# Kernel tuning notes

Measured on AMD Instinct MI355X. Metric: run time of the kernel, lower is better.

Reference implementation:

```python
import jax, jax.numpy as jnp
import numpy as np

MEMORY_LENGTH = 32   # past states remembered
N_TARGETS = 3        # leak sources
T_STEPS = 1000       # duration / dt
DT = 0.1
HIDDEN = 128         # policy MLP hidden width
N_AGENTS = 1024      # vmapped batch of rollouts
IN_DIM = MEMORY_LENGTH * 3 + MEMORY_LENGTH  # flattened x_hist + conc_hist


def setup_inputs() -> dict:
    key = jax.random.key(0)
    k0, k1, k2, k3, k4 = jax.random.split(key, 5)
    target_pos = jax.random.normal(k0, (N_TARGETS, 2), dtype=jnp.float32) * 5.0
    logsigma = jax.random.normal(k1, (N_TARGETS,), dtype=jnp.float32) * 0.5
    x_inits = jax.random.normal(k2, (N_AGENTS, 3), dtype=jnp.float32) * 2.0
    W1 = jax.random.normal(k3, (HIDDEN, IN_DIM), dtype=jnp.float32) / np.sqrt(IN_DIM).astype(np.float32)
    b1 = jnp.zeros((HIDDEN,), dtype=jnp.float32)
    W2 = jax.random.normal(k4, (2, HIDDEN), dtype=jnp.float32) / np.sqrt(HIDDEN).astype(np.float32)
    b2 = jnp.zeros((2,), dtype=jnp.float32)
    return {"target_pos": target_pos, "logsigma": logsigma, "x_inits": x_inits,
            "W1": W1, "b1": b1, "W2": W2, "b2": b2}


def _concentration(x, y, target_pos, sigma):
    # x, y: [N]; target_pos: [nt, 2]; sigma: [nt] -> conc: [N]
    d2 = (x[:, None] - target_pos[None, :, 0]) ** 2 + (y[:, None] - target_pos[None, :, 1]) ** 2
    return ((1.0 / sigma) * jnp.exp(-d2 / sigma)).sum(-1)


def reference(target_pos, logsigma, x_inits, W1, b1, W2, b2):
    sigma = jnp.exp(logsigma)
    N = x_inits.shape[0]
    # initial histories: memory_length copies of the initial state / concentration
    x_hist0 = jnp.tile(x_inits[:, None, :], (1, MEMORY_LENGTH, 1))        # [N, M, 3]
    conc0 = _concentration(x_inits[:, 0], x_inits[:, 1], target_pos, sigma)
    conc_hist0 = jnp.tile(conc0[:, None], (1, MEMORY_LENGTH))             # [N, M]

    def step(carry, _):
        x_hist, conc_hist, x_cur = carry
        # policy MLP on flattened histories -> tanh controls (v, omega)
        feats = jnp.concatenate([x_hist.reshape(N, -1), conc_hist], axis=-1)  # [N, 4M]
        h = jax.nn.relu(feats @ W1.T + b1)
        u = jnp.tanh(h @ W2.T + b2)                                            # [N, 2]
        v, w = u[:, 0], u[:, 1]
        th = x_cur[:, 2]
        # Dubins car dynamics (zero actuation noise)
        x_next = x_cur + DT * jnp.stack([v * jnp.cos(th), v * jnp.sin(th), w], axis=-1)
        # shift histories: drop oldest, insert newest at front
        x_hist = jnp.concatenate([x_next[:, None, :], x_hist[:, :-1, :]], axis=1)
        c = _concentration(x_next[:, 0], x_next[:, 1], target_pos, sigma)
        conc_hist = jnp.concatenate([c[:, None], conc_hist[:, :-1]], axis=1)
        return (x_hist, conc_hist, x_next), (x_next, u)

    _, (traj, ctrl) = jax.lax.scan(step, (x_hist0, conc_hist0, x_inits), None, length=T_STEPS)
    # traj: [T, N, 3], ctrl: [T, N, 2]
    d2 = ((traj[:, :, 0][..., None] - target_pos[None, None, :, 0]) ** 2
          + (traj[:, :, 1][..., None] - target_pos[None, None, :, 1]) ** 2)   # [T, N, nt]
    per_target = (-1.0 / sigma) * jnp.exp(-d2 / sigma)                        # [T, N, nt]
    cost = per_target.mean(axis=(0, 1)).sum() + (ctrl ** 2).mean()
    return cost
```

## Files before the change

kernel.cpp:

```cpp
#include <hip/hip_runtime.h>

#define T_STEPS 1000
#define DT 0.1f
#define HIDDEN 128
#define N_AGENTS 1024
#define U 2
#define RING (U + 16)

typedef float v2f __attribute__((ext_vector_type(2)));

__device__ __forceinline__ float tanh_fast(float x) {
    float e = __expf(2.0f * x);
    return 1.0f - 2.0f * __builtin_amdgcn_rcpf(e + 1.0f);
}

__device__ __forceinline__ v2f opaque_load8(const float* p) {
    v2f v;
    asm volatile("global_load_dwordx2 %0, %1, off\n\ts_waitcnt vmcnt(0)"
                 : "=v"(v)
                 : "v"((unsigned long long)(uintptr_t)p)
                 : "memory");
    return v;
}

__device__ __forceinline__ float uniformf(float v) {
    return __builtin_bit_cast(float,
        __builtin_amdgcn_readfirstlane(__builtin_bit_cast(int, v)));
}

__device__ __forceinline__ float wave_sum_dpp(float x) {
    float t;
    #define DPPADD(ctrl, rmask)                                              \
        t = __builtin_bit_cast(float, __builtin_amdgcn_update_dpp(           \
                0, __builtin_bit_cast(int, x), ctrl, rmask, 0xf, false));    \
        x += t;
    DPPADD(0x111, 0xf)
    DPPADD(0x112, 0xf)
    DPPADD(0x114, 0xf)
    DPPADD(0x118, 0xf)
    DPPADD(0x142, 0xa)
    DPPADD(0x143, 0xc)
    #undef DPPADD
    return __builtin_bit_cast(float,
        __builtin_amdgcn_readlane(__builtin_bit_cast(int, x), 63));
}

__global__ void pack_kernel(const float* __restrict__ W1,
                            float* __restrict__ pw) {
    const int row = blockIdx.x;
    const int a   = threadIdx.x;
    const float* rp = W1 + row * 128;
    float* out = pw + row * 128;
    out[2*a]          = rp[3*a];
    out[2*a + 1]      = rp[3*a + 1];
    out[64 + 2*a]     = rp[3*a + 2];
    out[64 + 2*a + 1] = rp[96 + a];
}

__global__ __launch_bounds__(128)
__attribute__((amdgpu_waves_per_eu(1, 2)))
void sim_kernel(const float* __restrict__ target_pos,
                const float* __restrict__ logsigma,
                const float* __restrict__ x_inits,
                const float* __restrict__ pw,
                const float* __restrict__ b1,
                const float* __restrict__ W2,
                const float* __restrict__ b2,
                float2* __restrict__ ws) {
    const int agent = blockIdx.x;
    const int tid  = threadIdx.x;
    const int h    = tid >> 6;
    const int lane = tid & 63;
    const int rowA = lane;
    const int rowB = lane + 64;

    __shared__ float2 part1[32][64];
    __shared__ alignas(16) float2 pbf[2];

    const float tx0 = uniformf(target_pos[0]), ty0 = uniformf(target_pos[1]);
    const float tx1 = uniformf(target_pos[2]), ty1 = uniformf(target_pos[3]);
    const float tx2 = uniformf(target_pos[4]), ty2 = uniformf(target_pos[5]);
    const float is0 = uniformf(1.0f / expf(logsigma[0]));
    const float is1 = uniformf(1.0f / expf(logsigma[1]));
    const float is2 = uniformf(1.0f / expf(logsigma[2]));

    v2f WxyA[16], WzcA[16], WxyB[16], WzcB[16];
    {
        const float* baseA = pw + rowA * 128;
        const float* baseB = pw + rowB * 128;
        #pragma unroll
        for (int i = 0; i < 16; ++i) {
            WxyA[i] = opaque_load8(baseA + 32 * h + 2 * i);
            WzcA[i] = opaque_load8(baseA + 64 + 32 * h + 2 * i);
            WxyB[i] = opaque_load8(baseB + 32 * h + 2 * i);
            WzcB[i] = opaque_load8(baseB + 64 + 32 * h + 2 * i);
        }
    }
    const float b1A = b1[rowA], b1B = b1[rowB];
    const float w20A = W2[rowA], w20B = W2[rowB];
    const float w21A = W2[HIDDEN + rowA], w21B = W2[HIDDEN + rowB];
    const float b2x = uniformf(b2[0]), b2y = uniformf(b2[1]);

    auto conc = [&](float px, float py) {
        float dx0 = px - tx0, dy0 = py - ty0;
        float dx1 = px - tx1, dy1 = py - ty1;
        float dx2 = px - tx2, dy2 = py - ty2;
        float cc  = is0 * __expf(-(dx0*dx0 + dy0*dy0) * is0);
        cc       += is1 * __expf(-(dx1*dx1 + dy1*dy1) * is1);
        cc       += is2 * __expf(-(dx2*dx2 + dy2*dy2) * is2);
        return cc;
    };

    float x  = uniformf(x_inits[3 * agent]);
    float y  = uniformf(x_inits[3 * agent + 1]);
    float th = uniformf(x_inits[3 * agent + 2]);
    float c  = conc(x, y);

    v2f RA[RING], RB[RING];
    #pragma unroll
    for (int i = 16; i < RING; ++i) { RA[i] = (v2f){0.f,0.f}; RB[i] = (v2f){0.f,0.f}; }
    {
        v2f exy = {x, y}, ezc = {th, c};
        v2f aA = {0.f, 0.f}, aB = {0.f, 0.f};
        #pragma unroll
        for (int k = 15; k >= 0; --k) {
            aA = WxyA[k] * exy + aA;  aA = WzcA[k] * ezc + aA;
            aB = WxyB[k] * exy + aB;  aB = WzcB[k] * ezc + aB;
            RA[k] = aA;  RB[k] = aB;
        }
    }
    if (h == 1) {
        float2 s0 = make_float2(RA[0].x + RA[0].y, RB[0].x + RB[0].y);
        #pragma unroll
        for (int s = 0; s < 16; ++s) part1[s][lane] = s0;
    }
    __syncthreads();

    float2 pl = part1[0][lane];
    float S_c = 0.f, S_u = 0.f;
    int t = 0;

    #pragma unroll 1
    for (int tt = 0; tt < T_STEPS / U; ++tt) {
        #pragma unroll
        for (int j = 0; j < U; ++j, ++t) {
            if (h == 0) {
                float hA = fmaxf((RA[j].x + RA[j].y) + pl.x + b1A, 0.f);
                float hB = fmaxf((RB[j].x + RB[j].y) + pl.y + b1B, 0.f);
                float s0 = wave_sum_dpp(fmaf(w20A, hA, w20B * hB));
                float s1 = wave_sum_dpp(fmaf(w21A, hA, w21B * hB));
                if (lane == 0) pbf[t & 1] = make_float2(s0, s1);
            } else {
                part1[(t + 16) & 31][lane] =
                    make_float2(RA[j].x + RA[j].y, RB[j].x + RB[j].y);
            }
            __syncthreads();

            pl = part1[(t + 1) & 31][lane];

            float2 pp = pbf[t & 1];
            float P0 = pp.x, P1 = pp.y;

            float v  = tanh_fast(P0 + b2x);
            float wv = tanh_fast(P1 + b2y);
            S_u += v * v + wv * wv;

            float sn = __sinf(th), cs = __cosf(th);
            float dv = DT * v;
            x  = fmaf(dv, cs, x);
            y  = fmaf(dv, sn, y);
            th = fmaf(DT, wv, th);

            c = conc(x, y);
            S_c += c;

            {
                v2f exy = {x, y}, ezc = {th, c};
                #pragma unroll
                for (int k = 0; k < 16; ++k) {
                    RA[j+1+k] = WxyA[k] * exy + RA[j+1+k];
                    RA[j+1+k] = WzcA[k] * ezc + RA[j+1+k];
                    RB[j+1+k] = WxyB[k] * exy + RB[j+1+k];
                    RB[j+1+k] = WzcB[k] * ezc + RB[j+1+k];
                }
            }
        }
        #pragma unroll
        for (int i = 0; i < 16; ++i) { RA[i] = RA[i + U]; RB[i] = RB[i + U]; }
        #pragma unroll
        for (int i = 16; i < RING; ++i) { RA[i] = (v2f){0.f,0.f}; RB[i] = (v2f){0.f,0.f}; }
    }

    if (tid == 0) ws[agent] = make_float2(S_c, S_u);
}

__global__ void reduce_kernel(const float2* __restrict__ ws,
                              float* __restrict__ out) {
    const int tid = threadIdx.x;
    float sc = 0.f, su = 0.f;
    for (int i = tid; i < N_AGENTS; i += 256) {
        float2 v = ws[i];
        sc += v.x;
        su += v.y;
    }
    #pragma unroll
    for (int off = 32; off > 0; off >>= 1) {
        sc += __shfl_xor(sc, off);
        su += __shfl_xor(su, off);
    }
    __shared__ float2 partw[4];
    int wave = tid >> 6;
    if ((tid & 63) == 0) partw[wave] = make_float2(sc, su);
    __syncthreads();
    if (tid == 0) {
        float SC = partw[0].x + partw[1].x + partw[2].x + partw[3].x;
        float SU = partw[0].y + partw[1].y + partw[2].y + partw[3].y;
        const float invNT  = 1.0f / (float)(N_AGENTS * T_STEPS);
        const float invNT2 = 1.0f / (float)(N_AGENTS * T_STEPS * 2);
        out[0] = -SC * invNT + SU * invNT2;
    }
}

extern "C" void kernel_launch(void* const* d_in, const int* in_sizes, int n_in,
                              void* d_out, int out_size, void* d_ws, size_t ws_size,
                              hipStream_t stream) {
    const float* target_pos = (const float*)d_in[0];
    const float* logsigma   = (const float*)d_in[1];
    const float* x_inits    = (const float*)d_in[2];
    const float* W1         = (const float*)d_in[3];
    const float* b1         = (const float*)d_in[4];
    const float* W2         = (const float*)d_in[5];
    const float* b2         = (const float*)d_in[6];

    float*  pw   = (float*)d_ws;
    float2* sums = (float2*)((char*)d_ws + 64 * 1024);

    pack_kernel<<<HIDDEN, 32, 0, stream>>>(W1, pw);
    sim_kernel<<<N_AGENTS, 128, 0, stream>>>(target_pos, logsigma, x_inits,
                                             pw, b1, W2, b2, sums);
    reduce_kernel<<<1, 256, 0, stream>>>(sums, (float*)d_out);
}
```

Before: 734.4 us.

## Split recurrence into a wave-specialised pipeline with a register ring buffer

The two waves get separate roles. Wave 0 runs the serial critical path (MLP head reduction, dynamics, concentration) and publishes the new state through a small LDS ring. Wave 1 lags behind, reads that state, and accumulates the older-history partial sums into LDS, so it no longer repeats wave 0's dynamics. The register accumulators become a 16-entry modular ring unrolled 16 ways, which removes the per-iteration shift and zeroing copies. The cost is a more intricate lag and indexing scheme between the waves, where an off-by-one would silently give wrong results, plus larger code size.

```diff
diff --git a/kernel.cpp b/kernel.cpp
--- a/kernel.cpp
+++ b/kernel.cpp
@@ -4,8 +4,6 @@
 #define DT 0.1f
 #define HIDDEN 128
 #define N_AGENTS 1024
-#define U 2
-#define RING (U + 16)
 
 typedef float v2f __attribute__((ext_vector_type(2)));
 
@@ -75,7 +73,7 @@
     const int rowB = lane + 64;
 
     __shared__ float2 part1[32][64];
-    __shared__ alignas(16) float2 pbf[2];
+    __shared__ float4 e4buf[4];
 
     const float tx0 = uniformf(target_pos[0]), ty0 = uniformf(target_pos[1]);
     const float tx1 = uniformf(target_pos[2]), ty1 = uniformf(target_pos[3]);
@@ -116,82 +114,116 @@
     float th = uniformf(x_inits[3 * agent + 2]);
     float c  = conc(x, y);
 
-    v2f RA[RING], RB[RING];
-    #pragma unroll
-    for (int i = 16; i < RING; ++i) { RA[i] = (v2f){0.f,0.f}; RB[i] = (v2f){0.f,0.f}; }
+    v2f RA[16], RB[16];
     {
-        v2f exy = {x, y}, ezc = {th, c};
-        v2f aA = {0.f, 0.f}, aB = {0.f, 0.f};
-        #pragma unroll
-        for (int k = 15; k >= 0; --k) {
-            aA = WxyA[k] * exy + aA;  aA = WzcA[k] * ezc + aA;
-            aB = WxyB[k] * exy + aB;  aB = WzcB[k] * ezc + aB;
-            RA[k] = aA;  RB[k] = aB;
-        }
-    }
-    if (h == 1) {
-        float2 s0 = make_float2(RA[0].x + RA[0].y, RB[0].x + RB[0].y);
-        #pragma unroll
-        for (int s = 0; s < 16; ++s) part1[s][lane] = s0;
+        v2f exy0 = {x, y}, ezc0 = {th, c};
+        if (h == 0) {
+            v2f aA = {0.f,0.f}, aB = {0.f,0.f};
+            #pragma unroll
+            for (int k = 15; k >= 0; --k) {
+                aA = WxyA[k]*exy0 + aA;  aA = WzcA[k]*ezc0 + aA;
+                aB = WxyB[k]*exy0 + aB;  aB = WzcB[k]*ezc0 + aB;
+                RA[k] = aA;  RB[k] = aB;
+            }
+            if (lane == 0) {
+                float4 e0 = make_float4(x, y, th, c);
+                e4buf[3] = e0;
+                e4buf[0] = e0;
+            }
+        } else {
+            v2f aA = {0.f,0.f}, aB = {0.f,0.f};
+            RA[14] = (v2f){0.f,0.f};  RB[14] = (v2f){0.f,0.f};
+            #pragma unroll
+            for (int k = 15; k >= 2; --k) {
+                aA = WxyA[k]*exy0 + aA;  aA = WzcA[k]*ezc0 + aA;
+                aB = WxyB[k]*exy0 + aB;  aB = WzcB[k]*ezc0 + aB;
+                RA[k-2] = aA;  RB[k-2] = aB;
+            }
+            aA = WxyA[1]*exy0 + aA;  aA = WzcA[1]*ezc0 + aA;
+            aB = WxyB[1]*exy0 + aB;  aB = WzcB[1]*ezc0 + aB;
+            RA[15] = aA;  RB[15] = aB;
+            v2f fA = WxyA[0]*exy0 + aA;  fA = WzcA[0]*ezc0 + fA;
+            v2f fB = WxyB[0]*exy0 + aB;  fB = WzcB[0]*ezc0 + fB;
+            float2 full = make_float2(fA.x + fA.y, fB.x + fB.y);
+            #pragma unroll
+            for (int s = 0; s < 16; ++s) part1[s][lane] = full;
+        }
     }
     __syncthreads();
 
-    float2 pl = part1[0][lane];
     float S_c = 0.f, S_u = 0.f;
-    int t = 0;
-
-    #pragma unroll 1
-    for (int tt = 0; tt < T_STEPS / U; ++tt) {
-        #pragma unroll
-        for (int j = 0; j < U; ++j, ++t) {
-            if (h == 0) {
-                float hA = fmaxf((RA[j].x + RA[j].y) + pl.x + b1A, 0.f);
-                float hB = fmaxf((RB[j].x + RB[j].y) + pl.y + b1B, 0.f);
-                float s0 = wave_sum_dpp(fmaf(w20A, hA, w20B * hB));
-                float s1 = wave_sum_dpp(fmaf(w21A, hA, w21B * hB));
-                if (lane == 0) pbf[t & 1] = make_float2(s0, s1);
-            } else {
-                part1[(t + 16) & 31][lane] =
-                    make_float2(RA[j].x + RA[j].y, RB[j].x + RB[j].y);
-            }
+
+    if (h == 0) {
+        float2 pl = part1[0][lane];
+        auto h0_step = [&](int t, int j) {
             __syncthreads();
-
-            pl = part1[(t + 1) & 31][lane];
-
-            float2 pp = pbf[t & 1];
-            float P0 = pp.x, P1 = pp.y;
-
-            float v  = tanh_fast(P0 + b2x);
-            float wv = tanh_fast(P1 + b2y);
+            float hA = fmaxf((RA[j].x + RA[j].y) + pl.x + b1A, 0.f);
+            float hB = fmaxf((RB[j].x + RB[j].y) + pl.y + b1B, 0.f);
+            float s0 = wave_sum_dpp(fmaf(w20A, hA, w20B * hB));
+            float s1 = wave_sum_dpp(fmaf(w21A, hA, w21B * hB));
+            float v  = tanh_fast(s0 + b2x);
+            float wv = tanh_fast(s1 + b2y);
             S_u += v * v + wv * wv;
-
             float sn = __sinf(th), cs = __cosf(th);
             float dv = DT * v;
             x  = fmaf(dv, cs, x);
             y  = fmaf(dv, sn, y);
             th = fmaf(DT, wv, th);
-
-            c = conc(x, y);
+            c  = conc(x, y);
             S_c += c;
-
+            if (lane == 0) e4buf[(t + 1) & 3] = make_float4(x, y, th, c);
+            v2f exy = {x, y}, ezc = {th, c};
+            RA[j] = WxyA[15] * exy;  RA[j] = WzcA[15] * ezc + RA[j];
+            RB[j] = WxyB[15] * exy;  RB[j] = WzcB[15] * ezc + RB[j];
+            #pragma unroll
+            for (int k = 0; k < 15; ++k) {
+                const int m = (j + 1 + k) & 15;
+                RA[m] = WxyA[k] * exy + RA[m];  RA[m] = WzcA[k] * ezc + RA[m];
+                RB[m] = WxyB[k] * exy + RB[m];  RB[m] = WzcB[k] * ezc + RB[m];
+            }
+            pl = part1[(t + 1) & 31][lane];
+        };
+        #pragma unroll 1
+        for (int tt = 0; tt < 62; ++tt) {
+            const int tb = tt * 16;
+            #pragma unroll
+            for (int j = 0; j < 16; ++j) h0_step(tb + j, j);
+        }
+        #pragma unroll
+        for (int j = 0; j < 8; ++j) h0_step(992 + j, j);
+
+        if (lane == 0) ws[agent] = make_float2(S_c, S_u);
+    } else {
+        auto h1_step = [&](int t, int j) {
+            __syncthreads();
+            float4 e = e4buf[(t - 1) & 3];
+            v2f exy = {e.x, e.y}, ezc = {e.z, e.w};
             {
-                v2f exy = {x, y}, ezc = {th, c};
-                #pragma unroll
-                for (int k = 0; k < 16; ++k) {
-                    RA[j+1+k] = WxyA[k] * exy + RA[j+1+k];
-                    RA[j+1+k] = WzcA[k] * ezc + RA[j+1+k];
-                    RB[j+1+k] = WxyB[k] * exy + RB[j+1+k];
-                    RB[j+1+k] = WzcB[k] * ezc + RB[j+1+k];
-                }
-            }
+                const int m = (j + 14) & 15;
+                RA[m] = WxyA[15] * exy;  RA[m] = WzcA[15] * ezc + RA[m];
+                RB[m] = WxyB[15] * exy;  RB[m] = WzcB[15] * ezc + RB[m];
+            }
+            #pragma unroll
+            for (int k = 0; k < 15; ++k) {
+                const int m = (j + 15 + k) & 15;
+                RA[m] = WxyA[k] * exy + RA[m];  RA[m] = WzcA[k] * ezc + RA[m];
+                RB[m] = WxyB[k] * exy + RB[m];  RB[m] = WzcB[k] * ezc + RB[m];
+            }
+            {
+                const int m = (j + 15) & 15;
+                part1[(t + 15) & 31][lane] =
+                    make_float2(RA[m].x + RA[m].y, RB[m].x + RB[m].y);
+            }
+        };
+        #pragma unroll 1
+        for (int tt = 0; tt < 62; ++tt) {
+            const int tb = tt * 16;
+            #pragma unroll
+            for (int j = 0; j < 16; ++j) h1_step(tb + j, j);
         }
         #pragma unroll
-        for (int i = 0; i < 16; ++i) { RA[i] = RA[i + U]; RB[i] = RB[i + U]; }
-        #pragma unroll
-        for (int i = 16; i < RING; ++i) { RA[i] = (v2f){0.f,0.f}; RB[i] = (v2f){0.f,0.f}; }
-    }
-
-    if (tid == 0) ws[agent] = make_float2(S_c, S_u);
+        for (int j = 0; j < 8; ++j) h1_step(992 + j, j);
+    }
 }
 
 __global__ void reduce_kernel(const float2* __restrict__ ws,
```

Measured after the change: 661.1 us. 1.11x faster.

## Collapse two-wave agent pipeline into single wave with full-history register ring

Applied to the files above, without the earlier changes.

Each agent now runs on one 64-lane wave instead of two. That wave holds all 32 memory slots of the W1 partial sums in registers and computes the whole hidden pre-activation itself. This removes the per-step __syncthreads and the LDS exchange of partial sums and policy outputs. The inner loop is also unrolled 8 steps per ring shift instead of 2. In exchange, each wave does twice the FMA work per step, and register pressure roughly doubles, from 128 weight regs plus a larger ring. That could spill or cut occupancy, though occupancy is already limited to one wave per EU.

```diff
diff --git a/kernel.cpp b/kernel.cpp
--- a/kernel.cpp
+++ b/kernel.cpp
@@ -4,19 +4,18 @@
 #define DT 0.1f
 #define HIDDEN 128
 #define N_AGENTS 1024
-#define U 2
-#define RING (U + 16)
 
 typedef float v2f __attribute__((ext_vector_type(2)));
+typedef float v4f __attribute__((ext_vector_type(4)));
 
 __device__ __forceinline__ float tanh_fast(float x) {
     float e = __expf(2.0f * x);
     return 1.0f - 2.0f * __builtin_amdgcn_rcpf(e + 1.0f);
 }
 
-__device__ __forceinline__ v2f opaque_load8(const float* p) {
-    v2f v;
-    asm volatile("global_load_dwordx2 %0, %1, off\n\ts_waitcnt vmcnt(0)"
+__device__ __forceinline__ v4f opaque_load16(const float* p) {
+    v4f v;
+    asm volatile("global_load_dwordx4 %0, %1, off\n\ts_waitcnt vmcnt(0)"
                  : "=v"(v)
                  : "v"((unsigned long long)(uintptr_t)p)
                  : "memory");
@@ -57,8 +56,8 @@
     out[64 + 2*a + 1] = rp[96 + a];
 }
 
-__global__ __launch_bounds__(128)
-__attribute__((amdgpu_waves_per_eu(1, 2)))
+__global__ __launch_bounds__(64)
+__attribute__((amdgpu_waves_per_eu(1, 1)))
 void sim_kernel(const float* __restrict__ target_pos,
                 const float* __restrict__ logsigma,
                 const float* __restrict__ x_inits,
@@ -68,14 +67,9 @@
                 const float* __restrict__ b2,
                 float2* __restrict__ ws) {
     const int agent = blockIdx.x;
-    const int tid  = threadIdx.x;
-    const int h    = tid >> 6;
-    const int lane = tid & 63;
-    const int rowA = lane;
-    const int rowB = lane + 64;
-
-    __shared__ float2 part1[32][64];
-    __shared__ alignas(16) float2 pbf[2];
+    const int lane  = threadIdx.x;
+    const int rowA  = lane;
+    const int rowB  = lane + 64;
 
     const float tx0 = uniformf(target_pos[0]), ty0 = uniformf(target_pos[1]);
     const float tx1 = uniformf(target_pos[2]), ty1 = uniformf(target_pos[3]);
@@ -84,16 +78,21 @@
     const float is1 = uniformf(1.0f / expf(logsigma[1]));
     const float is2 = uniformf(1.0f / expf(logsigma[2]));
 
-    v2f WxyA[16], WzcA[16], WxyB[16], WzcB[16];
+    v2f WxyA[32], WzcA[32], WxyB[32], WzcB[32];
     {
         const float* baseA = pw + rowA * 128;
         const float* baseB = pw + rowB * 128;
         #pragma unroll
         for (int i = 0; i < 16; ++i) {
-            WxyA[i] = opaque_load8(baseA + 32 * h + 2 * i);
-            WzcA[i] = opaque_load8(baseA + 64 + 32 * h + 2 * i);
-            WxyB[i] = opaque_load8(baseB + 32 * h + 2 * i);
-            WzcB[i] = opaque_load8(baseB + 64 + 32 * h + 2 * i);
+            v4f q;
+            q = opaque_load16(baseA + 4 * i);
+            WxyA[2*i] = q.xy;  WxyA[2*i+1] = q.zw;
+            q = opaque_load16(baseA + 64 + 4 * i);
+            WzcA[2*i] = q.xy;  WzcA[2*i+1] = q.zw;
+            q = opaque_load16(baseB + 4 * i);
+            WxyB[2*i] = q.xy;  WxyB[2*i+1] = q.zw;
+            q = opaque_load16(baseB + 64 + 4 * i);
+            WzcB[2*i] = q.xy;  WzcB[2*i+1] = q.zw;
         }
     }
     const float b1A = b1[rowA], b1B = b1[rowB];
@@ -116,82 +115,57 @@
     float th = uniformf(x_inits[3 * agent + 2]);
     float c  = conc(x, y);
 
-    v2f RA[RING], RB[RING];
-    #pragma unroll
-    for (int i = 16; i < RING; ++i) { RA[i] = (v2f){0.f,0.f}; RB[i] = (v2f){0.f,0.f}; }
+    v2f RA[40], RB[40];
     {
-        v2f exy = {x, y}, ezc = {th, c};
+        v2f exy0 = {x, y}, ezc0 = {th, c};
         v2f aA = {0.f, 0.f}, aB = {0.f, 0.f};
         #pragma unroll
-        for (int k = 15; k >= 0; --k) {
-            aA = WxyA[k] * exy + aA;  aA = WzcA[k] * ezc + aA;
-            aB = WxyB[k] * exy + aB;  aB = WzcB[k] * ezc + aB;
+        for (int k = 31; k >= 0; --k) {
+            aA = WxyA[k] * exy0 + aA;  aA = WzcA[k] * ezc0 + aA;
+            aB = WxyB[k] * exy0 + aB;  aB = WzcB[k] * ezc0 + aB;
             RA[k] = aA;  RB[k] = aB;
         }
-    }
-    if (h == 1) {
-        float2 s0 = make_float2(RA[0].x + RA[0].y, RB[0].x + RB[0].y);
-        #pragma unroll
-        for (int s = 0; s < 16; ++s) part1[s][lane] = s0;
-    }
-    __syncthreads();
-
-    float2 pl = part1[0][lane];
+        #pragma unroll
+        for (int i = 32; i < 40; ++i) { RA[i] = (v2f){0.f,0.f}; RB[i] = (v2f){0.f,0.f}; }
+    }
+
     float S_c = 0.f, S_u = 0.f;
-    int t = 0;
 
     #pragma unroll 1
-    for (int tt = 0; tt < T_STEPS / U; ++tt) {
-        #pragma unroll
-        for (int j = 0; j < U; ++j, ++t) {
-            if (h == 0) {
-                float hA = fmaxf((RA[j].x + RA[j].y) + pl.x + b1A, 0.f);
-                float hB = fmaxf((RB[j].x + RB[j].y) + pl.y + b1B, 0.f);
-                float s0 = wave_sum_dpp(fmaf(w20A, hA, w20B * hB));
-                float s1 = wave_sum_dpp(fmaf(w21A, hA, w21B * hB));
-                if (lane == 0) pbf[t & 1] = make_float2(s0, s1);
-            } else {
-                part1[(t + 16) & 31][lane] =
-                    make_float2(RA[j].x + RA[j].y, RB[j].x + RB[j].y);
-            }
-            __syncthreads();
-
-            pl = part1[(t + 1) & 31][lane];
-
-            float2 pp = pbf[t & 1];
-            float P0 = pp.x, P1 = pp.y;
-
-            float v  = tanh_fast(P0 + b2x);
-            float wv = tanh_fast(P1 + b2y);
+    for (int tt = 0; tt < 125; ++tt) {
+        #pragma unroll
+        for (int j = 0; j < 8; ++j) {
+            float hA = fmaxf((RA[j].x + RA[j].y) + b1A, 0.f);
+            float hB = fmaxf((RB[j].x + RB[j].y) + b1B, 0.f);
+            float s0 = wave_sum_dpp(fmaf(w20A, hA, w20B * hB));
+            float s1 = wave_sum_dpp(fmaf(w21A, hA, w21B * hB));
+
+            float v  = tanh_fast(s0 + b2x);
+            float wv = tanh_fast(s1 + b2y);
             S_u += v * v + wv * wv;
-
             float sn = __sinf(th), cs = __cosf(th);
             float dv = DT * v;
             x  = fmaf(dv, cs, x);
             y  = fmaf(dv, sn, y);
             th = fmaf(DT, wv, th);
-
-            c = conc(x, y);
+            c  = conc(x, y);
             S_c += c;
 
-            {
-                v2f exy = {x, y}, ezc = {th, c};
-                #pragma unroll
-                for (int k = 0; k < 16; ++k) {
-                    RA[j+1+k] = WxyA[k] * exy + RA[j+1+k];
-                    RA[j+1+k] = WzcA[k] * ezc + RA[j+1+k];
-                    RB[j+1+k] = WxyB[k] * exy + RB[j+1+k];
-                    RB[j+1+k] = WzcB[k] * ezc + RB[j+1+k];
-                }
+            v2f exy = {x, y}, ezc = {th, c};
+            #pragma unroll
+            for (int k = 0; k < 32; ++k) {
+                const int m = j + 1 + k;
+                RA[m] = WxyA[k] * exy + RA[m];  RA[m] = WzcA[k] * ezc + RA[m];
+                RB[m] = WxyB[k] * exy + RB[m];  RB[m] = WzcB[k] * ezc + RB[m];
             }
         }
         #pragma unroll
-        for (int i = 0; i < 16; ++i) { RA[i] = RA[i + U]; RB[i] = RB[i + U]; }
-        #pragma unroll
-        for (int i = 16; i < RING; ++i) { RA[i] = (v2f){0.f,0.f}; RB[i] = (v2f){0.f,0.f}; }
-    }
-
-    if (tid == 0) ws[agent] = make_float2(S_c, S_u);
+        for (int i = 0; i < 32; ++i) { RA[i] = RA[i + 8]; RB[i] = RB[i + 8]; }
+        #pragma unroll
+        for (int i = 32; i < 40; ++i) { RA[i] = (v2f){0.f,0.f}; RB[i] = (v2f){0.f,0.f}; }
+    }
+
+    if (lane == 0) ws[agent] = make_float2(S_c, S_u);
 }
 
 __global__ void reduce_kernel(const float2* __restrict__ ws,
@@ -236,7 +210,7 @@
     float2* sums = (float2*)((char*)d_ws + 64 * 1024);
 
     pack_kernel<<<HIDDEN, 32, 0, stream>>>(W1, pw);
-    sim_kernel<<<N_AGENTS, 128, 0, stream>>>(target_pos, logsigma, x_inits,
-                                             pw, b1, W2, b2, sums);
+    sim_kernel<<<N_AGENTS, 64, 0, stream>>>(target_pos, logsigma, x_inits,
+                                            pw, b1, W2, b2, sums);
     reduce_kernel<<<1, 256, 0, stream>>>(sums, (float*)d_out);
 }
```

Result: slower. 2.161 ms (+194.3%).
